# Kernel tuning notes

Measured on AMD Instinct MI355X. Metric: run time of the kernel, lower is better.

The kernel has to match this reference:

```python
import jax, jax.numpy as jnp
import numpy as np
import math

EPS = 1e-3          # self.eps
M = 0.5             # margin
H = 0.333           # rad_h
S = 64.0            # scale
HEAD_B = 0.5        # head_b
BATCH_MEAN = 0.0    # registered buffer initial value
BATCH_STD = 100.0   # registered buffer initial value
B, D, C = 1024, 512, 51332


def setup_inputs() -> dict:
    key = jax.random.key(0)
    k1, k2, k3, k4 = jax.random.split(key, 4)
    emb = jax.random.normal(k1, (B, D), dtype=jnp.float32)
    # face embeddings are typically l2-normalized before this head
    emb = emb / jnp.clip(jnp.linalg.norm(emb, axis=1, keepdims=True), 1e-5)
    # feature norms in a realistic range [5, 35)
    norms = jax.random.uniform(k2, (B, 1), dtype=jnp.float32) * 30.0 + 5.0
    kernel = jax.random.normal(k3, (D, C), dtype=jnp.float32)
    label = jax.random.randint(k4, (B,), 0, C)
    return {"embbedings": emb, "norms": norms, "kernel": kernel, "label": label}


def reference(embbedings, norms, kernel, label):
    # l2_norm(kernel, axis=0)
    kn = kernel / jnp.clip(jnp.linalg.norm(kernel, axis=0, keepdims=True), 1e-5)
    # [B, C] cosine logits
    cosine = jnp.clip(embbedings @ kn, -1.0 + EPS, 1.0 - EPS)
    # detached norm-based margin scaler ('batchnorm' branch)
    safe_norms = jax.lax.stop_gradient(jnp.clip(norms, 1e-3, 100.0))
    ms = jnp.clip((safe_norms - BATCH_MEAN) / (BATCH_STD + EPS) * H, -1.0, 1.0)[:, 0]  # [B]
    rows = jnp.arange(cosine.shape[0])
    # additive angular margin only at the label column (equivalent to the one-hot scatter)
    theta = jnp.arccos(cosine).at[rows, label].add(M * ms)
    cos_m = jnp.cos(jnp.clip(theta, EPS, math.pi - EPS))
    # subtractive cosine margin at the label column
    cos_m = cos_m.at[rows, label].add(-(HEAD_B - M * ms))
    return cos_m * S
```

## Files before the change

kernel.cpp:

```cpp
#include <hip/hip_runtime.h>
#include <hip/hip_bf16.h>
#include <math.h>

#define B_ROWS 1024
#define DDIM   512
#define CN     51332
#define CPAD   51456
#define EPSF   1e-3f
#define SCALE  64.0f
#define NT     8

typedef unsigned short ushort_t;
typedef short bf16x8 __attribute__((ext_vector_type(8)));
typedef float f32x4  __attribute__((ext_vector_type(4)));
typedef unsigned short us8 __attribute__((ext_vector_type(8)));
typedef unsigned short us4 __attribute__((ext_vector_type(4)));

static __device__ __forceinline__ unsigned short f2bf(float f) {
    unsigned int u = __float_as_uint(f);
    u += 0x7fffu + ((u >> 16) & 1u);
    return (unsigned short)(u >> 16);
}

__global__ __launch_bounds__(256) void colpass(const float* __restrict__ kern,
        ushort_t* __restrict__ kbT, float* __restrict__ partials) {
    __shared__ ushort_t tile[64 * 256];
    const int c0 = blockIdx.x * 64;
    const int d0 = blockIdx.y * 256;
    const int t  = threadIdx.x;
    const int colL = t & 63;
    const int dg   = t >> 6;
    const int gcol = c0 + colL;
    const bool valid = gcol < CN;
    const int swz = colL & 31;
    float s = 0.f;
#pragma unroll
    for (int h = 0; h < 2; ++h) {
        float v[32];
        const int dh = d0 + dg * 64 + h * 32;
#pragma unroll
        for (int j = 0; j < 32; ++j)
            v[j] = valid ? kern[(size_t)(dh + j) * CN + gcol] : 0.f;
#pragma unroll
        for (int jj = 0; jj < 4; ++jj) {
            us8 pk;
#pragma unroll
            for (int e = 0; e < 8; ++e) {
                const float x = v[jj * 8 + e];
                s += x * x;
                pk[e] = f2bf(x);
            }
            const int cj = dg * 8 + h * 4 + jj;
            *(us8*)&tile[colL * 256 + ((cj ^ swz) << 3)] = pk;
        }
    }
    partials[(size_t)(blockIdx.y * 4 + dg) * CPAD + gcol] = s;
    __syncthreads();
    const int lane = t & 63;
    const int u = lane & 31, ch = lane >> 5;
#pragma unroll
    for (int p = 0; p < 8; ++p) {
        const int cl = p * 8 + dg * 2 + ch;
        const us8 val = *(const us8*)&tile[cl * 256 + ((u ^ (cl & 31)) << 3)];
        *(us8*)&kbT[(size_t)(c0 + cl) * DDIM + d0 + u * 8] = val;
    }
}

__global__ void finnorm(const float* __restrict__ partials, float* __restrict__ inv_norm) {
    const int c = blockIdx.x * 256 + threadIdx.x;
    float s = 0.f;
#pragma unroll
    for (int k = 0; k < 8; ++k) s += partials[(size_t)k * CPAD + c];
    inv_norm[c] = 1.0f / fmaxf(sqrtf(s), 1e-5f);
}

__global__ void embcast(const float* __restrict__ emb, ushort_t* __restrict__ embb) {
    const int t = blockIdx.x * 256 + threadIdx.x;
    const float4 v = ((const float4*)emb)[t];
    us4 o; o[0] = f2bf(v.x); o[1] = f2bf(v.y); o[2] = f2bf(v.z); o[3] = f2bf(v.w);
    *(us4*)&embb[(size_t)t * 4] = o;
}

#define MFMA(d, va, vb) (d) = __builtin_amdgcn_mfma_f32_16x16x32_bf16((va), (vb), (d), 0, 0, 0)

#define STAGE16(gp, lp) __builtin_amdgcn_global_load_lds( \
    (__attribute__((address_space(1))) void*)(gp), \
    (__attribute__((address_space(3))) void*)(lp), 16, 0, 0)

#define STAGE(gl, sb, half, kstep) do { \
    const int rb_ = (half) * 128 + w * 16; \
    STAGE16((gl) + (size_t)rb_ * DDIM + (size_t)(kstep) * 64, &(sb)[rb_ * 64]); \
    STAGE16((gl) + (size_t)(rb_ + 8) * DDIM + (size_t)(kstep) * 64, &(sb)[(rb_ + 8) * 64]); \
} while (0)

__global__ __launch_bounds__(512, 2) void gemm_kernel(
        const ushort_t* __restrict__ embb, const ushort_t* __restrict__ kbT,
        const float* __restrict__ inv_norm, float* __restrict__ out) {
    __shared__ ushort_t smem[49152];

    const int tid  = threadIdx.x;
    const int lane = tid & 63;
    const int w    = tid >> 6;
    const int wm = w >> 1, wn = w & 1;
    const int lm = lane & 15, lq = lane >> 4;
    const int r8 = lane >> 3, c8 = lane & 7;

    const int bid = blockIdx.x;
    const int u   = (bid & 7) * 201 + (bid >> 3);
    const int m0  = (u & 3) * 256;
    const int n0  = (u >> 2) * 128;

    const ushort_t* gAl = embb + (size_t)(m0 + r8) * DDIM + ((c8 ^ r8) << 3);
    const ushort_t* gBl = kbT  + (size_t)(n0 + r8) * DDIM + ((c8 ^ r8) << 3);
    const int swz = lm & 7;
    const int ca0 = ((lq    ) ^ swz) << 3;
    const int ca1 = ((lq + 4) ^ swz) << 3;
    const int offA = (wm * 64 + lm) * 64;
    const int offB = (wn * 64 + lm) * 64;

    f32x4 acc[4][4];
#pragma unroll
    for (int i = 0; i < 4; ++i)
#pragma unroll
        for (int j = 0; j < 4; ++j) acc[i][j] = (f32x4){0.f, 0.f, 0.f, 0.f};

    ushort_t* A0 = smem;
    ushort_t* A1 = smem + 16384;
    ushort_t* B0 = smem + 32768;
    ushort_t* B1 = smem + 40960;

    STAGE(gAl, A0, 0, 0); STAGE(gAl, A0, 1, 0);
    STAGE(gBl, B0, 0, 0);
    STAGE(gAl, A1, 0, 1); STAGE(gAl, A1, 1, 1);
    asm volatile("s_waitcnt vmcnt(4)" ::: "memory");
    __builtin_amdgcn_s_barrier();
    __builtin_amdgcn_sched_barrier(0);

    bf16x8 a[4][2], b0[2][2], b1[2][2];

    for (int t = 0; t < NT; ++t) {
        const int cur = t & 1;
        ushort_t* Sa  = (cur == 0) ? A0 : A1;
        ushort_t* Sb  = (cur == 0) ? B0 : B1;
        ushort_t* SbN = (cur == 0) ? B1 : B0;
        const int kA = (t + 2) & 7;
        const int kB = (t + 1) & 7;

#pragma unroll
        for (int i = 0; i < 4; ++i) {
            a[i][0] = *(const bf16x8*)&Sa[offA + i * 1024 + ca0];
            a[i][1] = *(const bf16x8*)&Sa[offA + i * 1024 + ca1];
        }
#pragma unroll
        for (int j = 0; j < 2; ++j) {
            b0[j][0] = *(const bf16x8*)&Sb[offB + j * 1024 + ca0];
            b0[j][1] = *(const bf16x8*)&Sb[offB + j * 1024 + ca1];
        }
        STAGE(gBl, SbN, 0, kB);
        __builtin_amdgcn_s_barrier();
        __builtin_amdgcn_s_setprio(1);
#pragma unroll
        for (int i = 0; i < 4; ++i)
#pragma unroll
            for (int j = 0; j < 2; ++j) {
                MFMA(acc[i][j], a[i][0], b0[j][0]);
                MFMA(acc[i][j], a[i][1], b0[j][1]);
            }
        __builtin_amdgcn_s_setprio(0);
        __builtin_amdgcn_s_barrier();
        __builtin_amdgcn_sched_barrier(0);

#pragma unroll
        for (int j = 0; j < 2; ++j) {
            b1[j][0] = *(const bf16x8*)&Sb[offB + (j + 2) * 1024 + ca0];
            b1[j][1] = *(const bf16x8*)&Sb[offB + (j + 2) * 1024 + ca1];
        }
        STAGE(gAl, Sa, 0, kA); STAGE(gAl, Sa, 1, kA);
        __builtin_amdgcn_s_barrier();
        __builtin_amdgcn_s_setprio(1);
#pragma unroll
        for (int i = 0; i < 4; ++i)
#pragma unroll
            for (int j = 0; j < 2; ++j) {
                MFMA(acc[i][j + 2], a[i][0], b1[j][0]);
                MFMA(acc[i][j + 2], a[i][1], b1[j][1]);
            }
        __builtin_amdgcn_s_setprio(0);
        asm volatile("s_waitcnt vmcnt(4)" ::: "memory");
        __builtin_amdgcn_s_barrier();
        __builtin_amdgcn_sched_barrier(0);
    }

    asm volatile("s_waitcnt vmcnt(0)" ::: "memory");
    __syncthreads();

    float invn[4];
#pragma unroll
    for (int j = 0; j < 4; ++j) {
        const int col = n0 + wn * 64 + j * 16 + lm;
        invn[j] = (col < CN) ? inv_norm[col] : 0.f;
    }
    float* Ew = (float*)smem + w * 1024;
    const int rr = lane >> 4, cc = lane & 15;
#pragma unroll
    for (int i = 0; i < 4; ++i) {
#pragma unroll
        for (int j = 0; j < 4; ++j)
#pragma unroll
            for (int r = 0; r < 4; ++r) {
                const int row = lq * 4 + r;
                const int cs  = ((j * 16 + lm) + row * 4) & 63;
                float v = acc[i][j][r] * invn[j];
                v = fminf(fmaxf(v, -(1.0f - EPSF)), 1.0f - EPSF) * SCALE;
                Ew[row * 64 + cs] = v;
            }
#pragma unroll
        for (int rep = 0; rep < 4; ++rep) {
            const int row = rep * 4 + rr;
            const f32x4 v = *(const f32x4*)&Ew[row * 64 + ((cc + row) & 15) * 4];
            const int grow = m0 + wm * 64 + i * 16 + row;
            const int gcol = n0 + wn * 64 + cc * 4;
            if (gcol < CN)
                *(f32x4*)&out[(size_t)grow * CN + gcol] = v;
        }
    }
}

__global__ void fixup(const float* __restrict__ norms, const int* __restrict__ label,
                      float* __restrict__ out) {
    const int b = blockIdx.x * 256 + threadIdx.x;
    if (b >= B_ROWS) return;
    const int c = label[b];
    const float safe = fminf(fmaxf(norms[b], 1e-3f), 100.0f);
    const float ms = fminf(fmaxf(safe / (100.0f + 1e-3f) * 0.333f, -1.0f), 1.0f);
    const size_t idx = (size_t)b * CN + c;
    const float cosv = out[idx] * (1.0f / SCALE);
    float theta = acosf(cosv) + 0.5f * ms;
    theta = fminf(fmaxf(theta, EPSF), 3.14159265358979f - EPSF);
    out[idx] = (cosf(theta) - (0.5f - 0.5f * ms)) * SCALE;
}

extern "C" void kernel_launch(void* const* d_in, const int* in_sizes, int n_in,
                              void* d_out, int out_size, void* d_ws, size_t ws_size,
                              hipStream_t stream) {
    const float* emb   = (const float*)d_in[0];
    const float* norms = (const float*)d_in[1];
    const float* kern  = (const float*)d_in[2];
    const int*   label = (const int*)d_in[3];
    float* out = (float*)d_out;

    char* ws = (char*)d_ws;
    ushort_t* kbT = (ushort_t*)ws;
    size_t off = (size_t)CPAD * DDIM * 2;
    ushort_t* embb = (ushort_t*)(ws + off); off += (size_t)B_ROWS * DDIM * 2;
    float* inv_norm = (float*)(ws + off);   off += (size_t)CPAD * 4;
    float* partials = (float*)(ws + off);

    colpass<<<dim3(CPAD / 64, 2), 256, 0, stream>>>(kern, kbT, partials);
    embcast<<<dim3((B_ROWS * DDIM / 4) / 256), 256, 0, stream>>>(emb, embb);
    finnorm<<<dim3(CPAD / 256), 256, 0, stream>>>(partials, inv_norm);
    gemm_kernel<<<dim3(1608), 512, 0, stream>>>(embb, kbT, inv_norm, out);
    fixup<<<dim3(B_ROWS / 256 + 1), 256, 0, stream>>>(norms, label, out);
}
```

Before: 391.5 us.

## Shrink GEMM block tile to 128x128 for higher occupancy

Cuts the GEMM block tile from 256x128 to 128x128, with 8 waves arranged 2x4 so each wave holds a 64x32 accumulator. LDS drops to 64 KB per block, and launch bounds now request 4 blocks per CU, so more blocks can be resident to hide latency. The grid doubles to 3216 blocks with a new swizzle, and the epilogue transpose is rewritten for 32-column wave tiles. The trade-off is that each B tile is reloaded for twice as many row blocks, which raises global and LDS traffic and lowers MFMA work per load. The fixup launch grid is also trimmed by one unused block.

```diff
diff --git a/kernel.cpp b/kernel.cpp
--- a/kernel.cpp
+++ b/kernel.cpp
@@ -87,28 +87,28 @@
     (__attribute__((address_space(1))) void*)(gp), \
     (__attribute__((address_space(3))) void*)(lp), 16, 0, 0)
 
-#define STAGE(gl, sb, half, kstep) do { \
-    const int rb_ = (half) * 128 + w * 16; \
+#define STAGE(gl, sb, kstep) do { \
+    const int rb_ = w * 16; \
     STAGE16((gl) + (size_t)rb_ * DDIM + (size_t)(kstep) * 64, &(sb)[rb_ * 64]); \
     STAGE16((gl) + (size_t)(rb_ + 8) * DDIM + (size_t)(kstep) * 64, &(sb)[(rb_ + 8) * 64]); \
 } while (0)
 
-__global__ __launch_bounds__(512, 2) void gemm_kernel(
+__global__ __launch_bounds__(512, 4) void gemm_kernel(
         const ushort_t* __restrict__ embb, const ushort_t* __restrict__ kbT,
         const float* __restrict__ inv_norm, float* __restrict__ out) {
-    __shared__ ushort_t smem[49152];
+    __shared__ ushort_t smem[32768];
 
     const int tid  = threadIdx.x;
     const int lane = tid & 63;
     const int w    = tid >> 6;
-    const int wm = w >> 1, wn = w & 1;
+    const int wm = w >> 2, wn = w & 3;
     const int lm = lane & 15, lq = lane >> 4;
     const int r8 = lane >> 3, c8 = lane & 7;
 
     const int bid = blockIdx.x;
-    const int u   = (bid & 7) * 201 + (bid >> 3);
-    const int m0  = (u & 3) * 256;
-    const int n0  = (u >> 2) * 128;
+    const int u   = (bid & 7) * 402 + (bid >> 3);
+    const int m0  = (u & 7) * 128;
+    const int n0  = (u >> 3) * 128;
 
     const ushort_t* gAl = embb + (size_t)(m0 + r8) * DDIM + ((c8 ^ r8) << 3);
     const ushort_t* gBl = kbT  + (size_t)(n0 + r8) * DDIM + ((c8 ^ r8) << 3);
@@ -116,36 +116,35 @@
     const int ca0 = ((lq    ) ^ swz) << 3;
     const int ca1 = ((lq + 4) ^ swz) << 3;
     const int offA = (wm * 64 + lm) * 64;
-    const int offB = (wn * 64 + lm) * 64;
-
-    f32x4 acc[4][4];
+    const int offB = (wn * 32 + lm) * 64;
+
+    f32x4 acc[4][2];
 #pragma unroll
     for (int i = 0; i < 4; ++i)
 #pragma unroll
-        for (int j = 0; j < 4; ++j) acc[i][j] = (f32x4){0.f, 0.f, 0.f, 0.f};
+        for (int j = 0; j < 2; ++j) acc[i][j] = (f32x4){0.f, 0.f, 0.f, 0.f};
 
     ushort_t* A0 = smem;
-    ushort_t* A1 = smem + 16384;
-    ushort_t* B0 = smem + 32768;
-    ushort_t* B1 = smem + 40960;
-
-    STAGE(gAl, A0, 0, 0); STAGE(gAl, A0, 1, 0);
-    STAGE(gBl, B0, 0, 0);
-    STAGE(gAl, A1, 0, 1); STAGE(gAl, A1, 1, 1);
-    asm volatile("s_waitcnt vmcnt(4)" ::: "memory");
+    ushort_t* A1 = smem + 8192;
+    ushort_t* B0 = smem + 16384;
+    ushort_t* B1 = smem + 24576;
+
+    STAGE(gAl, A0, 0);
+    STAGE(gBl, B0, 0);
+    STAGE(gAl, A1, 1);
+    asm volatile("s_waitcnt vmcnt(2)" ::: "memory");
     __builtin_amdgcn_s_barrier();
     __builtin_amdgcn_sched_barrier(0);
 
-    bf16x8 a[4][2], b0[2][2], b1[2][2];
-
     for (int t = 0; t < NT; ++t) {
         const int cur = t & 1;
-        ushort_t* Sa  = (cur == 0) ? A0 : A1;
-        ushort_t* Sb  = (cur == 0) ? B0 : B1;
-        ushort_t* SbN = (cur == 0) ? B1 : B0;
+        ushort_t* Sa  = cur ? A1 : A0;
+        ushort_t* Sb  = cur ? B1 : B0;
+        ushort_t* SbN = cur ? B0 : B1;
         const int kA = (t + 2) & 7;
         const int kB = (t + 1) & 7;
 
+        bf16x8 a[4][2], b[2][2];
 #pragma unroll
         for (int i = 0; i < 4; ++i) {
             a[i][0] = *(const bf16x8*)&Sa[offA + i * 1024 + ca0];
@@ -153,40 +152,31 @@
         }
 #pragma unroll
         for (int j = 0; j < 2; ++j) {
-            b0[j][0] = *(const bf16x8*)&Sb[offB + j * 1024 + ca0];
-            b0[j][1] = *(const bf16x8*)&Sb[offB + j * 1024 + ca1];
-        }
-        STAGE(gBl, SbN, 0, kB);
+            b[j][0] = *(const bf16x8*)&Sb[offB + j * 1024 + ca0];
+            b[j][1] = *(const bf16x8*)&Sb[offB + j * 1024 + ca1];
+        }
+        STAGE(gBl, SbN, kB);
         __builtin_amdgcn_s_barrier();
         __builtin_amdgcn_s_setprio(1);
 #pragma unroll
-        for (int i = 0; i < 4; ++i)
-#pragma unroll
-            for (int j = 0; j < 2; ++j) {
-                MFMA(acc[i][j], a[i][0], b0[j][0]);
-                MFMA(acc[i][j], a[i][1], b0[j][1]);
-            }
+        for (int i = 0; i < 4; ++i) {
+            MFMA(acc[i][0], a[i][0], b[0][0]);
+            MFMA(acc[i][0], a[i][1], b[0][1]);
+        }
         __builtin_amdgcn_s_setprio(0);
         __builtin_amdgcn_s_barrier();
         __builtin_amdgcn_sched_barrier(0);
 
-#pragma unroll
-        for (int j = 0; j < 2; ++j) {
-            b1[j][0] = *(const bf16x8*)&Sb[offB + (j + 2) * 1024 + ca0];
-            b1[j][1] = *(const bf16x8*)&Sb[offB + (j + 2) * 1024 + ca1];
-        }
-        STAGE(gAl, Sa, 0, kA); STAGE(gAl, Sa, 1, kA);
+        STAGE(gAl, Sa, kA);
         __builtin_amdgcn_s_barrier();
         __builtin_amdgcn_s_setprio(1);
 #pragma unroll
-        for (int i = 0; i < 4; ++i)
-#pragma unroll
-            for (int j = 0; j < 2; ++j) {
-                MFMA(acc[i][j + 2], a[i][0], b1[j][0]);
-                MFMA(acc[i][j + 2], a[i][1], b1[j][1]);
-            }
+        for (int i = 0; i < 4; ++i) {
+            MFMA(acc[i][1], a[i][0], b[1][0]);
+            MFMA(acc[i][1], a[i][1], b[1][1]);
+        }
         __builtin_amdgcn_s_setprio(0);
-        asm volatile("s_waitcnt vmcnt(4)" ::: "memory");
+        asm volatile("s_waitcnt vmcnt(2)" ::: "memory");
         __builtin_amdgcn_s_barrier();
         __builtin_amdgcn_sched_barrier(0);
     }
@@ -194,32 +184,33 @@
     asm volatile("s_waitcnt vmcnt(0)" ::: "memory");
     __syncthreads();
 
-    float invn[4];
-#pragma unroll
-    for (int j = 0; j < 4; ++j) {
-        const int col = n0 + wn * 64 + j * 16 + lm;
+    float invn[2];
+#pragma unroll
+    for (int j = 0; j < 2; ++j) {
+        const int col = n0 + wn * 32 + j * 16 + lm;
         invn[j] = (col < CN) ? inv_norm[col] : 0.f;
     }
-    float* Ew = (float*)smem + w * 1024;
-    const int rr = lane >> 4, cc = lane & 15;
+    float* Ew = (float*)smem + w * 512;
 #pragma unroll
     for (int i = 0; i < 4; ++i) {
 #pragma unroll
-        for (int j = 0; j < 4; ++j)
+        for (int j = 0; j < 2; ++j)
 #pragma unroll
             for (int r = 0; r < 4; ++r) {
                 const int row = lq * 4 + r;
-                const int cs  = ((j * 16 + lm) + row * 4) & 63;
+                const int cs  = ((j * 16 + lm) + row * 4) & 31;
                 float v = acc[i][j][r] * invn[j];
                 v = fminf(fmaxf(v, -(1.0f - EPSF)), 1.0f - EPSF) * SCALE;
-                Ew[row * 64 + cs] = v;
+                Ew[row * 32 + cs] = v;
             }
 #pragma unroll
-        for (int rep = 0; rep < 4; ++rep) {
-            const int row = rep * 4 + rr;
-            const f32x4 v = *(const f32x4*)&Ew[row * 64 + ((cc + row) & 15) * 4];
+        for (int rep = 0; rep < 2; ++rep) {
+            const int idx = rep * 64 + lane;
+            const int row = idx >> 3, uu = idx & 7;
+            const int us_ = (uu + row) & 7;
+            const f32x4 v = *(const f32x4*)&Ew[row * 32 + us_ * 4];
             const int grow = m0 + wm * 64 + i * 16 + row;
-            const int gcol = n0 + wn * 64 + cc * 4;
+            const int gcol = n0 + wn * 32 + uu * 4;
             if (gcol < CN)
                 *(f32x4*)&out[(size_t)grow * CN + gcol] = v;
         }
@@ -259,6 +250,6 @@
     colpass<<<dim3(CPAD / 64, 2), 256, 0, stream>>>(kern, kbT, partials);
     embcast<<<dim3((B_ROWS * DDIM / 4) / 256), 256, 0, stream>>>(emb, embb);
     finnorm<<<dim3(CPAD / 256), 256, 0, stream>>>(partials, inv_norm);
-    gemm_kernel<<<dim3(1608), 512, 0, stream>>>(embb, kbT, inv_norm, out);
-    fixup<<<dim3(B_ROWS / 256 + 1), 256, 0, stream>>>(norms, label, out);
-}
+    gemm_kernel<<<dim3(3216), 512, 0, stream>>>(embb, kbT, inv_norm, out);
+    fixup<<<dim3(B_ROWS / 256), 256, 0, stream>>>(norms, label, out);
+}
```

Result: no change. 389.9 us (-0.4%).
